# Performance work log

Measured on AMD Instinct MI355X. Metric: run time of the kernel, lower is better.

## Reference

```python
import jax, jax.numpy as jnp
import numpy as np

B, S, D, H = 4, 2048, 1024, 16
DH = D // H  # head dim = 64

def setup_inputs() -> dict:
    key = jax.random.key(0)
    ks = jax.random.split(key, 11)
    sc = 0.02
    return {
        "Q": jax.random.normal(ks[0], (B, S, D), jnp.float32),
        "K": jax.random.normal(ks[1], (B, S, D), jnp.float32),
        "V": jax.random.normal(ks[2], (B, S, D), jnp.float32),
        "Wq": jax.random.normal(ks[3], (D, D), jnp.float32) * sc,
        "bq": jnp.zeros((D,), jnp.float32),
        "Wk": jax.random.normal(ks[4], (D, D), jnp.float32) * sc,
        "bk": jnp.zeros((D,), jnp.float32),
        "Wv": jax.random.normal(ks[5], (D, D), jnp.float32) * sc,
        "bv": jnp.zeros((D,), jnp.float32),
        "Wo": jax.random.normal(ks[6], (D, D), jnp.float32) * sc,
        "bo": jnp.zeros((D,), jnp.float32),
    }

def reference(Q, K, V, Wq, bq, Wk, bk, Wv, bv, Wo, bo):
    # Linear projections (torch nn.Linear: x @ W.T + b)
    def proj(x, W, b):
        y = x @ W.T + b                      # [B,S,D]
        return y.reshape(B, -1, H, DH).transpose(0, 2, 1, 3)  # [B,H,S,DH]
    q = proj(Q, Wq, bq)
    k = proj(K, Wk, bk)
    v = proj(V, Wv, bv)
    scores = jnp.einsum('bhqd,bhkd->bhqk', q, k) / jnp.sqrt(jnp.float32(DH))
    attn = jax.nn.softmax(scores, axis=-1)   # dropout p=0 -> identity
    ctx = jnp.einsum('bhqk,bhkd->bhqd', attn, v)
    ctx = ctx.transpose(0, 2, 1, 3).reshape(B, -1, D)
    return ctx @ Wo.T + bo
```

## Files before the change

kernel.cpp:

```cpp
#include <hip/hip_runtime.h>
#include <hip/hip_bf16.h>
#include <cmath>

constexpr int kB = 4;
constexpr int kS = 2048;
constexpr int kD = 1024;
constexpr int kH = 16;

typedef __attribute__((ext_vector_type(8))) short bf16x8;
typedef __attribute__((ext_vector_type(4))) float f32x4;
typedef __attribute__((ext_vector_type(4))) unsigned int u32x4;

__device__ __forceinline__ unsigned short f2bf(float f) {
  unsigned int u = __builtin_bit_cast(unsigned int, f);
  u = (u + 0x7fffu + ((u >> 16) & 1u)) >> 16;
  return (unsigned short)u;
}

__device__ __forceinline__ f32x4 mfma16(bf16x8 a, bf16x8 b, f32x4 c) {
  return __builtin_amdgcn_mfma_f32_16x16x32_bf16(a, b, c, 0, 0, 0);
}

#define GL16(gsrc, ldst)                                                      \
  __builtin_amdgcn_global_load_lds(                                           \
      (const __attribute__((address_space(1))) unsigned int*)(gsrc),          \
      (__attribute__((address_space(3))) unsigned int*)(ldst), 16, 0, 0)

#define CVTPK(dst, lo, hi)                                                    \
  asm("v_cvt_pk_bf16_f32 %0, %1, %2" : "=v"(dst) : "v"(lo), "v"(hi))

#define WAITV(n) asm volatile("s_waitcnt vmcnt(" #n ")" ::: "memory")

__global__ __launch_bounds__(256) void cvt_w(
    const float* __restrict__ w0, const float* __restrict__ w1,
    const float* __restrict__ w2, const float* __restrict__ w3,
    unsigned short* __restrict__ o0, unsigned short* __restrict__ o1,
    unsigned short* __restrict__ o2, unsigned short* __restrict__ o3) {
  __shared__ short Ls[8192];
  const float* src = blockIdx.y == 0 ? w0 : blockIdx.y == 1 ? w1
                   : blockIdx.y == 2 ? w2 : w3;
  unsigned short* dst = blockIdx.y == 0 ? o0 : blockIdx.y == 1 ? o1
                      : blockIdx.y == 2 ? o2 : o3;
  const int pn = blockIdx.x >> 4;
  const int t64 = blockIdx.x & 15;
  const int tid = threadIdx.x;

#pragma unroll
  for (int it = 0; it < 4; ++it) {
    const int u = it * 256 + tid;
    const int row = u >> 3, k8 = u & 7;
    const float* s = src + (size_t)(pn * 128 + row) * kD + t64 * 64 + k8 * 8;
    float4 a = *reinterpret_cast<const float4*>(s);
    float4 b = *reinterpret_cast<const float4*>(s + 4);
    bf16x8 v;
    v[0] = (short)f2bf(a.x); v[1] = (short)f2bf(a.y);
    v[2] = (short)f2bf(a.z); v[3] = (short)f2bf(a.w);
    v[4] = (short)f2bf(b.x); v[5] = (short)f2bf(b.y);
    v[6] = (short)f2bf(b.z); v[7] = (short)f2bf(b.w);
    *reinterpret_cast<bf16x8*>(&Ls[(k8 * 128 + (row ^ k8)) * 8]) = v;
  }
  __syncthreads();
#pragma unroll
  for (int it = 0; it < 4; ++it) {
    const int g = it * 256 + tid;
    const int ks8 = g >> 7, row = g & 127;
    bf16x8 v = *reinterpret_cast<const bf16x8*>(&Ls[(ks8 * 128 + (row ^ ks8)) * 8]);
    const size_t cg = (size_t)pn * 16384 + (size_t)(t64 * 2 + (ks8 >> 2)) * 512 +
                      (ks8 & 3) * 128 + row;
    *reinterpret_cast<bf16x8*>(dst + cg * 8) = v;
  }
}

__global__ __launch_bounds__(256, 2) void proj_gemm3(
    const float* __restrict__ Xq, const float* __restrict__ Xk,
    const float* __restrict__ Xv,
    const unsigned short* __restrict__ Wq, const unsigned short* __restrict__ Wk,
    const unsigned short* __restrict__ Wv,
    const float* __restrict__ bq, const float* __restrict__ bk,
    const float* __restrict__ bv,
    unsigned short* __restrict__ oq, unsigned short* __restrict__ ok,
    unsigned short* __restrict__ ov) {
  const int vmode = blockIdx.z;
  const float* X = vmode == 0 ? Xq : vmode == 1 ? Xk : Xv;
  const unsigned short* Wb = vmode == 0 ? Wq : vmode == 1 ? Wk : Wv;
  const float* bias = vmode == 0 ? bq : vmode == 1 ? bk : bv;
  unsigned short* out = vmode == 0 ? oq : vmode == 1 ? ok : ov;
  const float scale = vmode == 0 ? 0.18033688f : 1.0f;

  __shared__ float Af[3][128 * 32];
  __shared__ short Bt[3][128 * 32];
  const int tid = threadIdx.x;
  const int lane = tid & 63;
  const int w = tid >> 6;
  const int wr = w >> 1, wc = w & 1;
  const int lg = lane >> 4, lc = lane & 15;
  const long bm = (long)blockIdx.x * 128;
  const int pn = blockIdx.y;
  const long bn = (long)pn * 128;
  const int sw = lc & 7;

  auto stage = [&](int bset, int ks) {
    const int k0 = ks * 32;
#pragma unroll
    for (int it = 0; it < 4; ++it) {
      const int cb = it * 256 + w * 64;
      const int c = cb + lane;
      const int row = c >> 3, ch = c & 7;
      GL16(X + (bm + row) * kD + k0 + ((ch ^ (row & 7)) << 2), &Af[bset][cb * 4]);
    }
#pragma unroll
    for (int it = 0; it < 2; ++it) {
      const int cb = it * 256 + w * 64;
      GL16(Wb + ((size_t)pn * 16384 + (size_t)ks * 512 + cb + lane) * 8,
           &Bt[bset][cb * 8]);
    }
  };

  f32x4 acc[4][4] = {};
  stage(0, 0);
  stage(1, 1);
  WAITV(6);
  __builtin_amdgcn_s_barrier();
  __builtin_amdgcn_sched_barrier(0);
  int cur = 0;

  for (int ks = 0; ks < 32; ++ks) {
    if (ks + 2 < 32) {
      int b2 = cur + 2; if (b2 >= 3) b2 -= 3;
      stage(b2, ks + 2);
    }
    const float* Ac = &Af[cur][0];
    const short* Bc = &Bt[cur][0];

    bf16x8 af[4], bfr[4];
#pragma unroll
    for (int mi = 0; mi < 4; ++mi) {
      const int row = wr * 64 + mi * 16 + lc;
      f32x4 a0 = *reinterpret_cast<const f32x4*>(Ac + row * 32 + (((lg * 2) ^ sw) << 2));
      f32x4 a1 = *reinterpret_cast<const f32x4*>(Ac + row * 32 + (((lg * 2 + 1) ^ sw) << 2));
      unsigned u0, u1, u2, u3;
      CVTPK(u0, a0[0], a0[1]); CVTPK(u1, a0[2], a0[3]);
      CVTPK(u2, a1[0], a1[1]); CVTPK(u3, a1[2], a1[3]);
      u32x4 uu = {u0, u1, u2, u3};
      af[mi] = __builtin_bit_cast(bf16x8, uu);
    }
#pragma unroll
    for (int ni = 0; ni < 4; ++ni)
      bfr[ni] = *reinterpret_cast<const bf16x8*>(
          Bc + (lg * 128 + wc * 64 + ni * 16 + lc) * 8);
    __builtin_amdgcn_s_setprio(1);
#pragma unroll
    for (int mi = 0; mi < 4; ++mi)
#pragma unroll
      for (int ni = 0; ni < 4; ++ni)
        acc[mi][ni] = mfma16(af[mi], bfr[ni], acc[mi][ni]);
    __builtin_amdgcn_s_setprio(0);

    if (ks < 31) {
      if (ks + 2 < 32) WAITV(6); else WAITV(0);
      __builtin_amdgcn_s_barrier();
      __builtin_amdgcn_sched_barrier(0);
    }
    cur = cur + 1 == 3 ? 0 : cur + 1;
  }

#pragma unroll
  for (int mi = 0; mi < 4; ++mi) {
#pragma unroll
    for (int ni = 0; ni < 4; ++ni) {
      const int n = (int)bn + wc * 64 + ni * 16 + lc;
      const float bv = bias[n];
      const int h = n >> 6, dh = n & 63;
#pragma unroll
      for (int i = 0; i < 4; ++i) {
        const int m = (int)bm + wr * 64 + mi * 16 + lg * 4 + i;
        const int b = m >> 11, s = m & 2047;
        const float v = (acc[mi][ni][i] + bv) * scale;
        size_t idx;
        if (vmode == 2)
          idx = ((size_t)((b * kH + h) * 256 + (s >> 3))) * 512 + (size_t)dh * 8 + (s & 7);
        else if (vmode == 1)
          idx = ((size_t)((b * kH + h) * kS + s)) * 64 +
                (((dh >> 3) ^ ((s & 3) | (((s >> 3) & 1) << 2))) << 3) + (dh & 7);
        else
          idx = ((size_t)((b * kH + h) * kS + s)) * 64 + dh;
        out[idx] = f2bf(v);
      }
    }
  }
}

__global__ __launch_bounds__(256, 4) void attn_fwd(
    const unsigned short* __restrict__ qh,
    const unsigned short* __restrict__ khs,
    const unsigned short* __restrict__ vs,
    unsigned short* __restrict__ ctx) {
  __shared__ short Kb[2][4096];
  __shared__ short Vb[2][4096];

  const int tid = threadIdx.x;
  const int lane = tid & 63;
  const int w = tid >> 6;
  const int lg = lane >> 4, lc = lane & 15;
  const int bid = blockIdx.x;
  const int wg = (bid & 7) * 128 + (bid >> 3);
  const int qt = wg & 15;
  const int bh = wg >> 4;
  const int q0w = qt * 128 + w * 32;
  const size_t base = (size_t)bh * kS * 64;
  const int krl = 8 * (lc >> 2) + (lc & 3);
  const int kc = (lg ^ ((lc & 3) | (((lc >> 2) & 1) << 2))) << 3;

  const bf16x8 qa00 = *reinterpret_cast<const bf16x8*>(qh + base + (size_t)(q0w + lc) * 64 + lg * 8);
  const bf16x8 qa01 = *reinterpret_cast<const bf16x8*>(qh + base + (size_t)(q0w + lc) * 64 + 32 + lg * 8);
  const bf16x8 qa10 = *reinterpret_cast<const bf16x8*>(qh + base + (size_t)(q0w + 16 + lc) * 64 + lg * 8);
  const bf16x8 qa11 = *reinterpret_cast<const bf16x8*>(qh + base + (size_t)(q0w + 16 + lc) * 64 + 32 + lg * 8);

  f32x4 o0[4] = {}, o1[4] = {};
  float m0 = -INFINITY, l0 = 0.f;
  float m1 = -INFINITY, l1 = 0.f;

  auto stage = [&](int bset, int kv0) {
#pragma unroll
    for (int it = 0; it < 2; ++it) {
      const int cb = it * 256 + w * 64;
      GL16(khs + base + (size_t)kv0 * 64 + (size_t)(cb + lane) * 8, &Kb[bset][cb * 8]);
      GL16(vs + base + (size_t)kv0 * 64 + (size_t)(cb + lane) * 8, &Vb[bset][cb * 8]);
    }
  };

  stage(0, 0);
  __syncthreads();
  int cur = 0;

  for (int t = 0; t < 32; ++t) {
    if (t + 1 < 32) stage(cur ^ 1, (t + 1) * 64);
    const short* Kc = &Kb[cur][0];
    const short* Vc = &Vb[cur][0];

#pragma unroll
    for (int kv32 = 0; kv32 < 64; kv32 += 32) {
      f32x4 s00, s01, s10, s11;
      __builtin_amdgcn_s_setprio(1);
      {
        const short* kr = Kc + (kv32 + krl) * 64;
        bf16x8 ka = *reinterpret_cast<const bf16x8*>(kr + kc);
        bf16x8 kb = *reinterpret_cast<const bf16x8*>(kr + (kc ^ 32));
        f32x4 z0 = {}, z1 = {};
        z0 = mfma16(ka, qa00, z0); z0 = mfma16(kb, qa01, z0);
        z1 = mfma16(ka, qa10, z1); z1 = mfma16(kb, qa11, z1);
        s00 = z0; s10 = z1;
      }
      {
        const short* kr = Kc + (kv32 + krl + 4) * 64;
        bf16x8 ka = *reinterpret_cast<const bf16x8*>(kr + kc);
        bf16x8 kb = *reinterpret_cast<const bf16x8*>(kr + (kc ^ 32));
        f32x4 z0 = {}, z1 = {};
        z0 = mfma16(ka, qa00, z0); z0 = mfma16(kb, qa01, z0);
        z1 = mfma16(ka, qa10, z1); z1 = mfma16(kb, qa11, z1);
        s01 = z0; s11 = z1;
      }
      __builtin_amdgcn_s_setprio(0);

      bf16x8 pa0, pa1;
      {
        float cm = fmaxf(fmaxf(fmaxf(s00[0], s00[1]), fmaxf(s00[2], s00[3])),
                         fmaxf(fmaxf(s01[0], s01[1]), fmaxf(s01[2], s01[3])));
        cm = fmaxf(cm, __shfl_xor(cm, 16));
        cm = fmaxf(cm, __shfl_xor(cm, 32));
        if (__any(cm > m0 + 11.0f)) {
          float mn = fmaxf(m0, cm);
          float sc = __builtin_amdgcn_exp2f(m0 - mn);
          m0 = mn; l0 *= sc;
#pragma unroll
          for (int i = 0; i < 4; ++i) {
            float si = __shfl(sc, lg * 4 + i);
            o0[0][i] *= si; o0[1][i] *= si; o0[2][i] *= si; o0[3][i] *= si;
          }
        }
        float pA = __builtin_amdgcn_exp2f(s00[0] - m0);
        float pB = __builtin_amdgcn_exp2f(s00[1] - m0);
        float pC = __builtin_amdgcn_exp2f(s00[2] - m0);
        float pD = __builtin_amdgcn_exp2f(s00[3] - m0);
        float pE = __builtin_amdgcn_exp2f(s01[0] - m0);
        float pF = __builtin_amdgcn_exp2f(s01[1] - m0);
        float pG = __builtin_amdgcn_exp2f(s01[2] - m0);
        float pH = __builtin_amdgcn_exp2f(s01[3] - m0);
        float rs = ((pA + pB) + (pC + pD)) + ((pE + pF) + (pG + pH));
        rs += __shfl_xor(rs, 16);
        rs += __shfl_xor(rs, 32);
        l0 += rs;
        unsigned uA, uB, uC, uD;
        CVTPK(uA, pA, pB); CVTPK(uB, pC, pD);
        CVTPK(uC, pE, pF); CVTPK(uD, pG, pH);
        u32x4 uu = {uA, uB, uC, uD};
        pa0 = __builtin_bit_cast(bf16x8, uu);
      }
      {
        float cm = fmaxf(fmaxf(fmaxf(s10[0], s10[1]), fmaxf(s10[2], s10[3])),
                         fmaxf(fmaxf(s11[0], s11[1]), fmaxf(s11[2], s11[3])));
        cm = fmaxf(cm, __shfl_xor(cm, 16));
        cm = fmaxf(cm, __shfl_xor(cm, 32));
        if (__any(cm > m1 + 11.0f)) {
          float mn = fmaxf(m1, cm);
          float sc = __builtin_amdgcn_exp2f(m1 - mn);
          m1 = mn; l1 *= sc;
#pragma unroll
          for (int i = 0; i < 4; ++i) {
            float si = __shfl(sc, lg * 4 + i);
            o1[0][i] *= si; o1[1][i] *= si; o1[2][i] *= si; o1[3][i] *= si;
          }
        }
        float pA = __builtin_amdgcn_exp2f(s10[0] - m1);
        float pB = __builtin_amdgcn_exp2f(s10[1] - m1);
        float pC = __builtin_amdgcn_exp2f(s10[2] - m1);
        float pD = __builtin_amdgcn_exp2f(s10[3] - m1);
        float pE = __builtin_amdgcn_exp2f(s11[0] - m1);
        float pF = __builtin_amdgcn_exp2f(s11[1] - m1);
        float pG = __builtin_amdgcn_exp2f(s11[2] - m1);
        float pH = __builtin_amdgcn_exp2f(s11[3] - m1);
        float rs = ((pA + pB) + (pC + pD)) + ((pE + pF) + (pG + pH));
        rs += __shfl_xor(rs, 16);
        rs += __shfl_xor(rs, 32);
        l1 += rs;
        unsigned uA, uB, uC, uD;
        CVTPK(uA, pA, pB); CVTPK(uB, pC, pD);
        CVTPK(uC, pE, pF); CVTPK(uD, pG, pH);
        u32x4 uu = {uA, uB, uC, uD};
        pa1 = __builtin_bit_cast(bf16x8, uu);
      }

      __builtin_amdgcn_s_setprio(1);
#pragma unroll
      for (int f = 0; f < 4; ++f) {
        bf16x8 vb = *reinterpret_cast<const bf16x8*>(
            Vc + ((kv32 >> 3) + lg) * 512 + (f * 16 + lc) * 8);
        o0[f] = mfma16(pa0, vb, o0[f]);
        o1[f] = mfma16(pa1, vb, o1[f]);
      }
      __builtin_amdgcn_s_setprio(0);
    }
    __syncthreads();
    cur ^= 1;
  }

  const int b = bh >> 4, h = bh & 15;
#pragma unroll
  for (int i = 0; i < 4; ++i) {
    const float inv0 = 1.0f / __shfl(l0, lg * 4 + i);
    const float inv1 = 1.0f / __shfl(l1, lg * 4 + i);
    const int m0g = b * kS + q0w + lg * 4 + i;
    const int m1g = m0g + 16;
#pragma unroll
    for (int f = 0; f < 4; ++f) {
      const int d = h * 64 + f * 16 + lc;
      const size_t coff = (size_t)(d >> 5) * 512 + ((d >> 3) & 3) * 128;
      ctx[((size_t)(m0g >> 7) * 16384 + coff + (m0g & 127)) * 8 + (d & 7)] =
          f2bf(o0[f][i] * inv0);
      ctx[((size_t)(m1g >> 7) * 16384 + coff + (m1g & 127)) * 8 + (d & 7)] =
          f2bf(o1[f][i] * inv1);
    }
  }
}

__global__ __launch_bounds__(256, 3) void oproj_gemm2(
    const unsigned short* __restrict__ A, const unsigned short* __restrict__ Wb,
    const float* __restrict__ bias, float* __restrict__ out) {
  __shared__ short At[3][4096];
  __shared__ short Bt[3][4096];
  const int tid = threadIdx.x;
  const int lane = tid & 63;
  const int w = tid >> 6;
  const int wr = w >> 1, wc = w & 1;
  const int lg = lane >> 4, lc = lane & 15;
  const int pm = blockIdx.x;
  const int pn = blockIdx.y;
  const long bm = (long)pm * 128;
  const long bn = (long)pn * 128;

  auto stage = [&](int bset, int ks) {
#pragma unroll
    for (int it = 0; it < 2; ++it) {
      const int cb = it * 256 + w * 64;
      GL16(A + ((size_t)pm * 16384 + (size_t)ks * 512 + cb + lane) * 8,
           &At[bset][cb * 8]);
      GL16(Wb + ((size_t)pn * 16384 + (size_t)ks * 512 + cb + lane) * 8,
           &Bt[bset][cb * 8]);
    }
  };

  f32x4 acc[4][4] = {};
  stage(0, 0);
  stage(1, 1);
  WAITV(4);
  __builtin_amdgcn_s_barrier();
  __builtin_amdgcn_sched_barrier(0);
  int cur = 0;

  for (int ks = 0; ks < 32; ++ks) {
    if (ks + 2 < 32) {
      int b2 = cur + 2; if (b2 >= 3) b2 -= 3;
      stage(b2, ks + 2);
    }
    const short* Ac = &At[cur][0];
    const short* Bc = &Bt[cur][0];
    bf16x8 af[4], bfr[4];
#pragma unroll
    for (int mi = 0; mi < 4; ++mi)
      af[mi] = *reinterpret_cast<const bf16x8*>(Ac + (lg * 128 + wr * 64 + mi * 16 + lc) * 8);
#pragma unroll
    for (int ni = 0; ni < 4; ++ni)
      bfr[ni] = *reinterpret_cast<const bf16x8*>(Bc + (lg * 128 + wc * 64 + ni * 16 + lc) * 8);
    __builtin_amdgcn_s_setprio(1);
#pragma unroll
    for (int mi = 0; mi < 4; ++mi)
#pragma unroll
      for (int ni = 0; ni < 4; ++ni)
        acc[mi][ni] = mfma16(af[mi], bfr[ni], acc[mi][ni]);
    __builtin_amdgcn_s_setprio(0);

    if (ks < 31) {
      if (ks + 2 < 32) WAITV(4); else WAITV(0);
      __builtin_amdgcn_s_barrier();
      __builtin_amdgcn_sched_barrier(0);
    }
    cur = cur + 1 == 3 ? 0 : cur + 1;
  }

#pragma unroll
  for (int mi = 0; mi < 4; ++mi) {
#pragma unroll
    for (int ni = 0; ni < 4; ++ni) {
      const int n = (int)bn + wc * 64 + ni * 16 + lc;
      const float bv = bias[n];
#pragma unroll
      for (int i = 0; i < 4; ++i) {
        const long m = bm + wr * 64 + mi * 16 + lg * 4 + i;
        out[(size_t)m * kD + n] = acc[mi][ni][i] + bv;
      }
    }
  }
}

extern "C" void kernel_launch(void* const* d_in, const int* in_sizes, int n_in,
                              void* d_out, int out_size, void* d_ws, size_t ws_size,
                              hipStream_t stream) {
  const float* Q  = (const float*)d_in[0];
  const float* K  = (const float*)d_in[1];
  const float* V  = (const float*)d_in[2];
  const float* Wq = (const float*)d_in[3];
  const float* bq = (const float*)d_in[4];
  const float* Wk = (const float*)d_in[5];
  const float* bk = (const float*)d_in[6];
  const float* Wv = (const float*)d_in[7];
  const float* bv = (const float*)d_in[8];
  const float* Wo = (const float*)d_in[9];
  const float* bo = (const float*)d_in[10];
  float* out = (float*)d_out;

  const size_t n_tok = (size_t)kB * kS * kD;
  const size_t n_w = (size_t)kD * kD;
  unsigned short* qh  = (unsigned short*)d_ws;
  unsigned short* kh  = qh + n_tok;
  unsigned short* vsw = kh + n_tok;
  unsigned short* cx  = vsw + n_tok;
  unsigned short* wqb = cx + n_tok;
  unsigned short* wkb = wqb + n_w;
  unsigned short* wvb = wkb + n_w;
  unsigned short* wob = wvb + n_w;

  dim3 blk(256, 1, 1);
  cvt_w<<<dim3(128, 4, 1), blk, 0, stream>>>(Wq, Wk, Wv, Wo, wqb, wkb, wvb, wob);
  proj_gemm3<<<dim3(64, 8, 3), blk, 0, stream>>>(Q, K, V, wqb, wkb, wvb,
                                                 bq, bk, bv, qh, kh, vsw);
  attn_fwd<<<dim3(1024, 1, 1), blk, 0, stream>>>(qh, kh, vsw, cx);
  oproj_gemm2<<<dim3(64, 8, 1), blk, 0, stream>>>(cx, wob, bo, out);
}
```

Baseline: 232.4 us.

## Pre-convert activations to bf16 and use 256x128 tiles with 512-thread GEMM blocks

Activations Q/K/V are now converted to bf16 in a tiled layout by an extended conversion kernel that also handles the weights, so the projection GEMM loads bf16 for both operands instead of converting fp32 in the inner loop. The projection and output GEMMs move to 512-thread blocks with 256x128 output tiles, double buffering and plain __syncthreads in place of the triple buffer with explicit vmcnt waits. This removes per-iteration conversion work and halves the fp32 activation bytes staged through shared memory in the GEMM. In exchange it adds an extra full pass that writes and rereads the activations, and a shallower prefetch pipeline.

Result: no change. 231.4 us (-0.4%).

```diff
diff --git a/kernel.cpp b/kernel.cpp
--- a/kernel.cpp
+++ b/kernel.cpp
@@ -29,18 +29,22 @@
 #define CVTPK(dst, lo, hi)                                                    \
   asm("v_cvt_pk_bf16_f32 %0, %1, %2" : "=v"(dst) : "v"(lo), "v"(hi))
 
-#define WAITV(n) asm volatile("s_waitcnt vmcnt(" #n ")" ::: "memory")
-
-__global__ __launch_bounds__(256) void cvt_w(
+__global__ __launch_bounds__(256) void cvt_all(
     const float* __restrict__ w0, const float* __restrict__ w1,
     const float* __restrict__ w2, const float* __restrict__ w3,
-    unsigned short* __restrict__ o0, unsigned short* __restrict__ o1,
-    unsigned short* __restrict__ o2, unsigned short* __restrict__ o3) {
-  __shared__ short Ls[8192];
-  const float* src = blockIdx.y == 0 ? w0 : blockIdx.y == 1 ? w1
-                   : blockIdx.y == 2 ? w2 : w3;
-  unsigned short* dst = blockIdx.y == 0 ? o0 : blockIdx.y == 1 ? o1
-                      : blockIdx.y == 2 ? o2 : o3;
+    const float* __restrict__ x0, const float* __restrict__ x1,
+    const float* __restrict__ x2,
+    unsigned short* __restrict__ ow0, unsigned short* __restrict__ ow1,
+    unsigned short* __restrict__ ow2, unsigned short* __restrict__ ow3,
+    unsigned short* __restrict__ ox0, unsigned short* __restrict__ ox1,
+    unsigned short* __restrict__ ox2) {
+  const int y = blockIdx.y;
+  if (y < 4 && blockIdx.x >= 128) return;
+  const float* src = y == 0 ? w0 : y == 1 ? w1 : y == 2 ? w2 : y == 3 ? w3
+                   : y == 4 ? x0 : y == 5 ? x1 : x2;
+  unsigned short* dst = y == 0 ? ow0 : y == 1 ? ow1 : y == 2 ? ow2 : y == 3 ? ow3
+                      : y == 4 ? ox0 : y == 5 ? ox1 : ox2;
+  __shared__ short Ls[128][72];
   const int pn = blockIdx.x >> 4;
   const int t64 = blockIdx.x & 15;
   const int tid = threadIdx.x;
@@ -57,23 +61,23 @@
     v[2] = (short)f2bf(a.z); v[3] = (short)f2bf(a.w);
     v[4] = (short)f2bf(b.x); v[5] = (short)f2bf(b.y);
     v[6] = (short)f2bf(b.z); v[7] = (short)f2bf(b.w);
-    *reinterpret_cast<bf16x8*>(&Ls[(k8 * 128 + (row ^ k8)) * 8]) = v;
+    *reinterpret_cast<bf16x8*>(&Ls[row][k8 * 8]) = v;
   }
   __syncthreads();
 #pragma unroll
   for (int it = 0; it < 4; ++it) {
     const int g = it * 256 + tid;
     const int ks8 = g >> 7, row = g & 127;
-    bf16x8 v = *reinterpret_cast<const bf16x8*>(&Ls[(ks8 * 128 + (row ^ ks8)) * 8]);
+    bf16x8 v = *reinterpret_cast<const bf16x8*>(&Ls[row][ks8 * 8]);
     const size_t cg = (size_t)pn * 16384 + (size_t)(t64 * 2 + (ks8 >> 2)) * 512 +
                       (ks8 & 3) * 128 + row;
     *reinterpret_cast<bf16x8*>(dst + cg * 8) = v;
   }
 }
 
-__global__ __launch_bounds__(256, 2) void proj_gemm3(
-    const float* __restrict__ Xq, const float* __restrict__ Xk,
-    const float* __restrict__ Xv,
+__global__ __launch_bounds__(512, 4) void proj_gemm4(
+    const unsigned short* __restrict__ Xq, const unsigned short* __restrict__ Xk,
+    const unsigned short* __restrict__ Xv,
     const unsigned short* __restrict__ Wq, const unsigned short* __restrict__ Wk,
     const unsigned short* __restrict__ Wv,
     const float* __restrict__ bq, const float* __restrict__ bk,
@@ -81,68 +85,52 @@
     unsigned short* __restrict__ oq, unsigned short* __restrict__ ok,
     unsigned short* __restrict__ ov) {
   const int vmode = blockIdx.z;
-  const float* X = vmode == 0 ? Xq : vmode == 1 ? Xk : Xv;
+  const unsigned short* X = vmode == 0 ? Xq : vmode == 1 ? Xk : Xv;
   const unsigned short* Wb = vmode == 0 ? Wq : vmode == 1 ? Wk : Wv;
   const float* bias = vmode == 0 ? bq : vmode == 1 ? bk : bv;
   unsigned short* out = vmode == 0 ? oq : vmode == 1 ? ok : ov;
   const float scale = vmode == 0 ? 0.18033688f : 1.0f;
 
-  __shared__ float Af[3][128 * 32];
-  __shared__ short Bt[3][128 * 32];
+  __shared__ short Alds[2][8192];
+  __shared__ short Blds[2][4096];
   const int tid = threadIdx.x;
   const int lane = tid & 63;
   const int w = tid >> 6;
   const int wr = w >> 1, wc = w & 1;
   const int lg = lane >> 4, lc = lane & 15;
-  const long bm = (long)blockIdx.x * 128;
+  const int pm = blockIdx.x;
   const int pn = blockIdx.y;
-  const long bn = (long)pn * 128;
-  const int sw = lc & 7;
-
-  auto stage = [&](int bset, int ks) {
-    const int k0 = ks * 32;
-#pragma unroll
-    for (int it = 0; it < 4; ++it) {
-      const int cb = it * 256 + w * 64;
+
+  auto stage = [&](int bs, int ks) {
+#pragma unroll
+    for (int it = 0; it < 2; ++it) {
+      const int cb = it * 512 + w * 64;
       const int c = cb + lane;
-      const int row = c >> 3, ch = c & 7;
-      GL16(X + (bm + row) * kD + k0 + ((ch ^ (row & 7)) << 2), &Af[bset][cb * 4]);
-    }
-#pragma unroll
-    for (int it = 0; it < 2; ++it) {
-      const int cb = it * 256 + w * 64;
+      GL16(X + ((size_t)(2 * pm + (c >> 9)) * 16384 + (size_t)ks * 512 + (c & 511)) * 8,
+           &Alds[bs][cb * 8]);
+    }
+    {
+      const int cb = w * 64;
       GL16(Wb + ((size_t)pn * 16384 + (size_t)ks * 512 + cb + lane) * 8,
-           &Bt[bset][cb * 8]);
+           &Blds[bs][cb * 8]);
     }
   };
 
   f32x4 acc[4][4] = {};
   stage(0, 0);
-  stage(1, 1);
-  WAITV(6);
-  __builtin_amdgcn_s_barrier();
-  __builtin_amdgcn_sched_barrier(0);
+  __syncthreads();
   int cur = 0;
 
   for (int ks = 0; ks < 32; ++ks) {
-    if (ks + 2 < 32) {
-      int b2 = cur + 2; if (b2 >= 3) b2 -= 3;
-      stage(b2, ks + 2);
-    }
-    const float* Ac = &Af[cur][0];
-    const short* Bc = &Bt[cur][0];
-
+    if (ks + 1 < 32) stage(cur ^ 1, ks + 1);
+    const short* Ac = &Alds[cur][0];
+    const short* Bc = &Blds[cur][0];
     bf16x8 af[4], bfr[4];
 #pragma unroll
     for (int mi = 0; mi < 4; ++mi) {
-      const int row = wr * 64 + mi * 16 + lc;
-      f32x4 a0 = *reinterpret_cast<const f32x4*>(Ac + row * 32 + (((lg * 2) ^ sw) << 2));
-      f32x4 a1 = *reinterpret_cast<const f32x4*>(Ac + row * 32 + (((lg * 2 + 1) ^ sw) << 2));
-      unsigned u0, u1, u2, u3;
-      CVTPK(u0, a0[0], a0[1]); CVTPK(u1, a0[2], a0[3]);
-      CVTPK(u2, a1[0], a1[1]); CVTPK(u3, a1[2], a1[3]);
-      u32x4 uu = {u0, u1, u2, u3};
-      af[mi] = __builtin_bit_cast(bf16x8, uu);
+      const int r = wr * 64 + mi * 16 + lc;
+      af[mi] = *reinterpret_cast<const bf16x8*>(
+          Ac + ((r >> 7) * 512 + lg * 128 + (r & 127)) * 8);
     }
 #pragma unroll
     for (int ni = 0; ni < 4; ++ni)
@@ -155,25 +143,20 @@
       for (int ni = 0; ni < 4; ++ni)
         acc[mi][ni] = mfma16(af[mi], bfr[ni], acc[mi][ni]);
     __builtin_amdgcn_s_setprio(0);
-
-    if (ks < 31) {
-      if (ks + 2 < 32) WAITV(6); else WAITV(0);
-      __builtin_amdgcn_s_barrier();
-      __builtin_amdgcn_sched_barrier(0);
-    }
-    cur = cur + 1 == 3 ? 0 : cur + 1;
+    __syncthreads();
+    cur ^= 1;
   }
 
 #pragma unroll
   for (int mi = 0; mi < 4; ++mi) {
 #pragma unroll
     for (int ni = 0; ni < 4; ++ni) {
-      const int n = (int)bn + wc * 64 + ni * 16 + lc;
+      const int n = pn * 128 + wc * 64 + ni * 16 + lc;
       const float bv = bias[n];
       const int h = n >> 6, dh = n & 63;
 #pragma unroll
       for (int i = 0; i < 4; ++i) {
-        const int m = (int)bm + wr * 64 + mi * 16 + lg * 4 + i;
+        const int m = pm * 256 + wr * 64 + mi * 16 + lg * 4 + i;
         const int b = m >> 11, s = m & 2047;
         const float v = (acc[mi][ni][i] + bv) * scale;
         size_t idx;
@@ -363,11 +346,11 @@
   }
 }
 
-__global__ __launch_bounds__(256, 3) void oproj_gemm2(
+__global__ __launch_bounds__(512, 4) void oproj_gemm4(
     const unsigned short* __restrict__ A, const unsigned short* __restrict__ Wb,
     const float* __restrict__ bias, float* __restrict__ out) {
-  __shared__ short At[3][4096];
-  __shared__ short Bt[3][4096];
+  __shared__ short Alds[2][8192];
+  __shared__ short Blds[2][4096];
   const int tid = threadIdx.x;
   const int lane = tid & 63;
   const int w = tid >> 6;
@@ -375,42 +358,42 @@
   const int lg = lane >> 4, lc = lane & 15;
   const int pm = blockIdx.x;
   const int pn = blockIdx.y;
-  const long bm = (long)pm * 128;
-  const long bn = (long)pn * 128;
-
-  auto stage = [&](int bset, int ks) {
+
+  auto stage = [&](int bs, int ks) {
 #pragma unroll
     for (int it = 0; it < 2; ++it) {
-      const int cb = it * 256 + w * 64;
-      GL16(A + ((size_t)pm * 16384 + (size_t)ks * 512 + cb + lane) * 8,
-           &At[bset][cb * 8]);
+      const int cb = it * 512 + w * 64;
+      const int c = cb + lane;
+      GL16(A + ((size_t)(2 * pm + (c >> 9)) * 16384 + (size_t)ks * 512 + (c & 511)) * 8,
+           &Alds[bs][cb * 8]);
+    }
+    {
+      const int cb = w * 64;
       GL16(Wb + ((size_t)pn * 16384 + (size_t)ks * 512 + cb + lane) * 8,
-           &Bt[bset][cb * 8]);
+           &Blds[bs][cb * 8]);
     }
   };
 
   f32x4 acc[4][4] = {};
   stage(0, 0);
-  stage(1, 1);
-  WAITV(4);
-  __builtin_amdgcn_s_barrier();
-  __builtin_amdgcn_sched_barrier(0);
+  __syncthreads();
   int cur = 0;
 
   for (int ks = 0; ks < 32; ++ks) {
-    if (ks + 2 < 32) {
-      int b2 = cur + 2; if (b2 >= 3) b2 -= 3;
-      stage(b2, ks + 2);
-    }
-    const short* Ac = &At[cur][0];
-    const short* Bc = &Bt[cur][0];
+    if (ks + 1 < 32) stage(cur ^ 1, ks + 1);
+    const short* Ac = &Alds[cur][0];
+    const short* Bc = &Blds[cur][0];
     bf16x8 af[4], bfr[4];
 #pragma unroll
-    for (int mi = 0; mi < 4; ++mi)
-      af[mi] = *reinterpret_cast<const bf16x8*>(Ac + (lg * 128 + wr * 64 + mi * 16 + lc) * 8);
+    for (int mi = 0; mi < 4; ++mi) {
+      const int r = wr * 64 + mi * 16 + lc;
+      af[mi] = *reinterpret_cast<const bf16x8*>(
+          Ac + ((r >> 7) * 512 + lg * 128 + (r & 127)) * 8);
+    }
 #pragma unroll
     for (int ni = 0; ni < 4; ++ni)
-      bfr[ni] = *reinterpret_cast<const bf16x8*>(Bc + (lg * 128 + wc * 64 + ni * 16 + lc) * 8);
+      bfr[ni] = *reinterpret_cast<const bf16x8*>(
+          Bc + (lg * 128 + wc * 64 + ni * 16 + lc) * 8);
     __builtin_amdgcn_s_setprio(1);
 #pragma unroll
     for (int mi = 0; mi < 4; ++mi)
@@ -418,24 +401,19 @@
       for (int ni = 0; ni < 4; ++ni)
         acc[mi][ni] = mfma16(af[mi], bfr[ni], acc[mi][ni]);
     __builtin_amdgcn_s_setprio(0);
-
-    if (ks < 31) {
-      if (ks + 2 < 32) WAITV(4); else WAITV(0);
-      __builtin_amdgcn_s_barrier();
-      __builtin_amdgcn_sched_barrier(0);
-    }
-    cur = cur + 1 == 3 ? 0 : cur + 1;
+    __syncthreads();
+    cur ^= 1;
   }
 
 #pragma unroll
   for (int mi = 0; mi < 4; ++mi) {
 #pragma unroll
     for (int ni = 0; ni < 4; ++ni) {
-      const int n = (int)bn + wc * 64 + ni * 16 + lc;
+      const int n = pn * 128 + wc * 64 + ni * 16 + lc;
       const float bv = bias[n];
 #pragma unroll
       for (int i = 0; i < 4; ++i) {
-        const long m = bm + wr * 64 + mi * 16 + lg * 4 + i;
+        const long m = (long)pm * 256 + wr * 64 + mi * 16 + lg * 4 + i;
         out[(size_t)m * kD + n] = acc[mi][ni][i] + bv;
       }
     }
@@ -463,16 +441,20 @@
   unsigned short* qh  = (unsigned short*)d_ws;
   unsigned short* kh  = qh + n_tok;
   unsigned short* vsw = kh + n_tok;
-  unsigned short* cx  = vsw + n_tok;
-  unsigned short* wqb = cx + n_tok;
+  unsigned short* xq  = vsw + n_tok;
+  unsigned short* xk  = xq + n_tok;
+  unsigned short* xv  = xk + n_tok;
+  unsigned short* wqb = xv + n_tok;
   unsigned short* wkb = wqb + n_w;
   unsigned short* wvb = wkb + n_w;
   unsigned short* wob = wvb + n_w;
-
-  dim3 blk(256, 1, 1);
-  cvt_w<<<dim3(128, 4, 1), blk, 0, stream>>>(Wq, Wk, Wv, Wo, wqb, wkb, wvb, wob);
-  proj_gemm3<<<dim3(64, 8, 3), blk, 0, stream>>>(Q, K, V, wqb, wkb, wvb,
-                                                 bq, bk, bv, qh, kh, vsw);
-  attn_fwd<<<dim3(1024, 1, 1), blk, 0, stream>>>(qh, kh, vsw, cx);
-  oproj_gemm2<<<dim3(64, 8, 1), blk, 0, stream>>>(cx, wob, bo, out);
-}
+  unsigned short* cx  = xq;
+
+  dim3 b256(256, 1, 1), b512(512, 1, 1);
+  cvt_all<<<dim3(1024, 7, 1), b256, 0, stream>>>(Wq, Wk, Wv, Wo, Q, K, V,
+                                                 wqb, wkb, wvb, wob, xq, xk, xv);
+  proj_gemm4<<<dim3(32, 8, 3), b512, 0, stream>>>(xq, xk, xv, wqb, wkb, wvb,
+                                                  bq, bk, bv, qh, kh, vsw);
+  attn_fwd<<<dim3(1024, 1, 1), b256, 0, stream>>>(qh, kh, vsw, cx);
+  oproj_gemm4<<<dim3(32, 8, 1), b512, 0, stream>>>(cx, wob, bo, out);
+}
```
